# Kernel tuning notes

Measured on AMD Instinct MI355X. Metric: run time of the kernel, lower is better.

Reference implementation:

```python
import jax, jax.numpy as jnp
import numpy as np

N, C, K = 100000, 64, 27
EPS = 1e-5


def setup_inputs() -> dict:
    key = jax.random.key(0)
    ks = jax.random.split(key, 8)
    feats = jax.random.normal(ks[0], (N, C), dtype=jnp.float32)
    W1 = jax.random.normal(ks[1], (K, C, C), dtype=jnp.float32) * (1.0 / np.sqrt(K * C))
    W2 = jax.random.normal(ks[2], (K, C, C), dtype=jnp.float32) * (1.0 / np.sqrt(K * C))
    gamma1 = jnp.ones((C,), dtype=jnp.float32)
    beta1 = jnp.zeros((C,), dtype=jnp.float32)
    gamma2 = jnp.ones((C,), dtype=jnp.float32)
    beta2 = jnp.zeros((C,), dtype=jnp.float32)
    nbr_idx1 = jax.random.randint(ks[3], (K, N), 0, N, dtype=jnp.int32)
    nbr_idx2 = jax.random.randint(ks[4], (K, N), 0, N, dtype=jnp.int32)
    nbr_mask1 = (jax.random.uniform(ks[5], (K, N)) < 0.7).astype(jnp.float32)
    nbr_mask2 = (jax.random.uniform(ks[6], (K, N)) < 0.7).astype(jnp.float32)
    return {"feats": feats, "W1": W1, "gamma1": gamma1, "beta1": beta1,
            "W2": W2, "gamma2": gamma2, "beta2": beta2,
            "nbr_idx1": nbr_idx1, "nbr_mask1": nbr_mask1,
            "nbr_idx2": nbr_idx2, "nbr_mask2": nbr_mask2}


def sparse_conv(f, idx, mask, W):
    # gather per kernel offset: [K, N, C], mask out missing neighbors
    g = f[idx] * mask[..., None]
    # per-offset GEMM and accumulate over offsets -> [N, C_out]
    return jnp.einsum('knc,kcd->nd', g, W)


def batch_norm(x, gamma, beta):
    # MinkowskiBatchNorm (training): stats over all N points, per channel
    mean = jnp.mean(x, axis=0)
    var = jnp.mean(jnp.square(x - mean), axis=0)
    return (x - mean) * jax.lax.rsqrt(var + EPS) * gamma + beta


def reference(feats, W1, gamma1, beta1, W2, gamma2, beta2,
              nbr_idx1, nbr_mask1, nbr_idx2, nbr_mask2):
    out = sparse_conv(feats, nbr_idx1, nbr_mask1, W1)
    out = jax.nn.relu(batch_norm(out, gamma1, beta1))
    out = sparse_conv(out, nbr_idx2, nbr_mask2, W2)
    out = batch_norm(out, gamma2, beta2)
    out = out + feats          # identity residual (stride=1, no downsample)
    return jax.nn.relu(out)
```

## Files before the change

### kernel.cpp

```cpp
#include <hip/hip_runtime.h>
#include <hip/hip_bf16.h>
#include <stdint.h>
#include <stddef.h>

#define N_PTS 100000
#define KOFF 27

typedef __attribute__((ext_vector_type(8))) __bf16 bf16x8;
typedef __attribute__((ext_vector_type(4))) float f32x4;

__device__ inline unsigned short f2bf(float f) {
  union { float f; unsigned u; } x; x.f = f;
  unsigned r = x.u + 0x7fffu + ((x.u >> 16) & 1u);
  return (unsigned short)(r >> 16);
}

__global__ __launch_bounds__(256) void prep_kernel(const float* __restrict__ feats,
                                                   const float* __restrict__ W1,
                                                   const float* __restrict__ W2,
                                                   unsigned short* __restrict__ featsb,
                                                   unsigned short* __restrict__ f2b,
                                                   unsigned short* __restrict__ wf1,
                                                   unsigned short* __restrict__ wf2,
                                                   float* __restrict__ stats) {
  __shared__ float sW[4096];
  int t = threadIdx.x;
  if (blockIdx.x < 54) {
    int which = blockIdx.x & 1;
    int k = blockIdx.x >> 1;
    const float* W = (which ? W2 : W1) + (size_t)k * 4096;
    unsigned short* wf = (which ? wf2 : wf1) + (size_t)k * 4096;
#pragma unroll
    for (int i = 0; i < 4; ++i)
      ((float4*)sW)[t + 256 * i] = ((const float4*)W)[t + 256 * i];
    __syncthreads();
#pragma unroll
    for (int i = 0; i < 16; ++i) {
      int o = i * 256 + t;
      int j = o & 7, l = (o >> 3) & 63, nt = (o >> 9) & 3, kk = (o >> 11) & 1;
      int c = kk * 32 + ((l >> 4) << 3) + j;
      int d = nt * 16 + (l & 15);
      wf[o] = f2bf(sW[c * 64 + d]);
    }
    return;
  }
  int fb = blockIdx.x - 54;
  int NB = gridDim.x - 54;
  const int NF4 = N_PTS * 16;
  for (int i = fb * 256 + t; i < NF4; i += NB * 256) {
    float4 v = ((const float4*)feats)[i];
    ushort4 o;
    o.x = f2bf(v.x); o.y = f2bf(v.y); o.z = f2bf(v.z); o.w = f2bf(v.w);
    ((ushort4*)featsb)[i] = o;
  }
  if (fb == 0) {
    if (t < 256) stats[t] = 0.f;
    uint4 z = make_uint4(0u, 0u, 0u, 0u);
    if (t < 8)            ((uint4*)(featsb + (size_t)N_PTS * 64))[t] = z;
    if (t >= 8 && t < 16) ((uint4*)(f2b    + (size_t)N_PTS * 64))[t - 8] = z;
  }
}

#define MFMA16(a, b, c) __builtin_amdgcn_mfma_f32_16x16x32_bf16(__builtin_bit_cast(bf16x8, a), __builtin_bit_cast(bf16x8, b), c, 0, 0, 0)

#define STEP(Ac0, Ac1, An0, An1, giN, mN, giF, mF, kcur)                        \
  {                                                                             \
    const uint4* bp = wfv + (size_t)(kcur) * 512 + lane;                        \
    uint4 b0 = bp[0],   b1 = bp[64],  b2 = bp[128], b3 = bp[192];               \
    uint4 b4 = bp[256], b5 = bp[320], b6 = bp[384], b7 = bp[448];               \
    {                                                                           \
      int gie = (mN != 0.f) ? giN : N_PTS;                                      \
      const char* rp = (const char*)fin + (size_t)gie * 128 + g16;              \
      An0 = *(const uint4*)rp;                                                  \
      An1 = *(const uint4*)(rp + 64);                                           \
    }                                                                           \
    {                                                                           \
      int kf = ((kcur) + 2 <= 26) ? (kcur) + 2 : 26;                            \
      giF = idxp[(size_t)kf * N_PTS];                                           \
      float mt = mp[(size_t)kf * N_PTS];                                        \
      mF = valid ? mt : 0.f;                                                    \
    }                                                                           \
    a0 = MFMA16(Ac0, b0, a0);                                                   \
    a1 = MFMA16(Ac0, b1, a1);                                                   \
    a2 = MFMA16(Ac0, b2, a2);                                                   \
    a3 = MFMA16(Ac0, b3, a3);                                                   \
    a0 = MFMA16(Ac1, b4, a0);                                                   \
    a1 = MFMA16(Ac1, b5, a1);                                                   \
    a2 = MFMA16(Ac1, b6, a2);                                                   \
    a3 = MFMA16(Ac1, b7, a3);                                                   \
  }

__global__ __launch_bounds__(256, 4) void conv_kernel(
    const unsigned short* __restrict__ fin,
    const unsigned short* __restrict__ wf,
    const int* __restrict__ idx,
    const float* __restrict__ mask,
    float* __restrict__ yout,
    float* __restrict__ gsum,
    float* __restrict__ gsq)
{
  int lane = threadIdx.x & 63;
  int wid  = threadIdx.x >> 6;
  int m    = lane & 15;
  int g    = lane >> 4;
  int g16  = g * 16;
  int n0   = blockIdx.x * 64 + wid * 16;
  int n    = n0 + m;
  bool valid = n < N_PTS;
  int nc = valid ? n : (N_PTS - 1);

  const int*   idxp = idx + nc;
  const float* mp   = mask + nc;
  const uint4* wfv  = (const uint4*)wf;

  f32x4 a0, a1, a2, a3;
#pragma unroll
  for (int r = 0; r < 4; ++r) { a0[r] = 0.f; a1[r] = 0.f; a2[r] = 0.f; a3[r] = 0.f; }

  uint4 Aa0, Aa1, Ab0, Ab1;
  int gi_a, gi_b; float m_a, m_b;

  gi_a = idxp[0];
  { float mt = mp[0]; m_a = valid ? mt : 0.f; }
  {
    int gie = (m_a != 0.f) ? gi_a : N_PTS;
    const char* rp = (const char*)fin + (size_t)gie * 128 + g16;
    Aa0 = *(const uint4*)rp;
    Aa1 = *(const uint4*)(rp + 64);
  }
  gi_b = idxp[N_PTS];
  { float mt = mp[N_PTS]; m_b = valid ? mt : 0.f; }

  for (int kk = 0; kk < 13; ++kk) {
    int k = 2 * kk;
    STEP(Aa0, Aa1, Ab0, Ab1, gi_b, m_b, gi_a, m_a, k);
    STEP(Ab0, Ab1, Aa0, Aa1, gi_a, m_a, gi_b, m_b, k + 1);
  }
  {
    const uint4* bp = wfv + (size_t)26 * 512 + lane;
    uint4 b0 = bp[0],   b1 = bp[64],  b2 = bp[128], b3 = bp[192];
    uint4 b4 = bp[256], b5 = bp[320], b6 = bp[384], b7 = bp[448];
    a0 = MFMA16(Aa0, b0, a0);
    a1 = MFMA16(Aa0, b1, a1);
    a2 = MFMA16(Aa0, b2, a2);
    a3 = MFMA16(Aa0, b3, a3);
    a0 = MFMA16(Aa1, b4, a0);
    a1 = MFMA16(Aa1, b5, a1);
    a2 = MFMA16(Aa1, b6, a2);
    a3 = MFMA16(Aa1, b7, a3);
  }

  __shared__ float s_sum[64], s_sq[64];
  if (threadIdx.x < 64) { s_sum[threadIdx.x] = 0.f; s_sq[threadIdx.x] = 0.f; }
  __syncthreads();

  float s0 = 0.f, q0 = 0.f, s1 = 0.f, q1 = 0.f, s2 = 0.f, q2 = 0.f, s3 = 0.f, q3 = 0.f;
#pragma unroll
  for (int r = 0; r < 4; ++r) {
    int row = n0 + g * 4 + r;
    bool rv = row < N_PTS;
    float v0 = a0[r]; s0 += v0; q0 += v0 * v0;
    float v1 = a1[r]; s1 += v1; q1 += v1 * v1;
    float v2 = a2[r]; s2 += v2; q2 += v2 * v2;
    float v3 = a3[r]; s3 += v3; q3 += v3 * v3;
    if (rv) {
      float* yr = yout + (size_t)row * 64;
      yr[m]      = v0;
      yr[16 + m] = v1;
      yr[32 + m] = v2;
      yr[48 + m] = v3;
    }
  }
  atomicAdd(&s_sum[m],      s0); atomicAdd(&s_sq[m],      q0);
  atomicAdd(&s_sum[16 + m], s1); atomicAdd(&s_sq[16 + m], q1);
  atomicAdd(&s_sum[32 + m], s2); atomicAdd(&s_sq[32 + m], q2);
  atomicAdd(&s_sum[48 + m], s3); atomicAdd(&s_sq[48 + m], q3);
  __syncthreads();
  if (threadIdx.x < 64) {
    atomicAdd(&gsum[threadIdx.x], s_sum[threadIdx.x]);
    atomicAdd(&gsq[threadIdx.x],  s_sq[threadIdx.x]);
  }
}

__global__ void bn1_kernel(const float* __restrict__ y,
                           const float* __restrict__ sum,
                           const float* __restrict__ sq,
                           const float* __restrict__ gamma,
                           const float* __restrict__ beta,
                           unsigned short* __restrict__ outb) {
  __shared__ float s_scale[64], s_shift[64];
  if (threadIdx.x < 64) {
    int c = threadIdx.x;
    float mean = sum[c] * (1.f / N_PTS);
    float var  = sq[c] * (1.f / N_PTS) - mean * mean;
    float inv  = rsqrtf(var + 1e-5f);
    float sc   = gamma[c] * inv;
    s_scale[c] = sc;
    s_shift[c] = beta[c] - mean * sc;
  }
  __syncthreads();
  int tid = blockIdx.x * blockDim.x + threadIdx.x;
  int stride = gridDim.x * blockDim.x;
  const int NT = N_PTS * 16;
  for (int i = tid; i < NT; i += stride) {
    float4 v = ((const float4*)y)[i];
    int c = (i * 4) & 63;
    float r0 = fmaxf(v.x * s_scale[c]     + s_shift[c],     0.f);
    float r1 = fmaxf(v.y * s_scale[c + 1] + s_shift[c + 1], 0.f);
    float r2 = fmaxf(v.z * s_scale[c + 2] + s_shift[c + 2], 0.f);
    float r3 = fmaxf(v.w * s_scale[c + 3] + s_shift[c + 3], 0.f);
    ushort4 o;
    o.x = f2bf(r0); o.y = f2bf(r1); o.z = f2bf(r2); o.w = f2bf(r3);
    ((ushort4*)outb)[i] = o;
  }
}

__global__ void bn2_kernel(const float* __restrict__ y,
                           const float* __restrict__ sum,
                           const float* __restrict__ sq,
                           const float* __restrict__ gamma,
                           const float* __restrict__ beta,
                           const float* __restrict__ feats,
                           float* __restrict__ out) {
  __shared__ float s_scale[64], s_shift[64];
  if (threadIdx.x < 64) {
    int c = threadIdx.x;
    float mean = sum[c] * (1.f / N_PTS);
    float var  = sq[c] * (1.f / N_PTS) - mean * mean;
    float inv  = rsqrtf(var + 1e-5f);
    float sc   = gamma[c] * inv;
    s_scale[c] = sc;
    s_shift[c] = beta[c] - mean * sc;
  }
  __syncthreads();
  int tid = blockIdx.x * blockDim.x + threadIdx.x;
  int stride = gridDim.x * blockDim.x;
  const int NT = N_PTS * 16;
  for (int i = tid; i < NT; i += stride) {
    float4 v = ((const float4*)y)[i];
    float4 f = ((const float4*)feats)[i];
    int c = (i * 4) & 63;
    float4 o;
    o.x = fmaxf(v.x * s_scale[c]     + s_shift[c]     + f.x, 0.f);
    o.y = fmaxf(v.y * s_scale[c + 1] + s_shift[c + 1] + f.y, 0.f);
    o.z = fmaxf(v.z * s_scale[c + 2] + s_shift[c + 2] + f.z, 0.f);
    o.w = fmaxf(v.w * s_scale[c + 3] + s_shift[c + 3] + f.w, 0.f);
    ((float4*)out)[i] = o;
  }
}

extern "C" void kernel_launch(void* const* d_in, const int* in_sizes, int n_in,
                              void* d_out, int out_size, void* d_ws, size_t ws_size,
                              hipStream_t stream) {
  const float* feats  = (const float*)d_in[0];
  const float* W1     = (const float*)d_in[1];
  const float* gamma1 = (const float*)d_in[2];
  const float* beta1  = (const float*)d_in[3];
  const float* W2     = (const float*)d_in[4];
  const float* gamma2 = (const float*)d_in[5];
  const float* beta2  = (const float*)d_in[6];
  const int*   idx1   = (const int*)d_in[7];
  const float* mask1  = (const float*)d_in[8];
  const int*   idx2   = (const int*)d_in[9];
  const float* mask2  = (const float*)d_in[10];
  float* out = (float*)d_out;

  char* ws = (char*)d_ws;
  unsigned short* featsb = (unsigned short*)(ws + 0);
  unsigned short* wf1    = (unsigned short*)(ws + 12800768);
  unsigned short* wf2    = (unsigned short*)(ws + 13021952);
  float*          stats  = (float*)(ws + 13243136);
  unsigned short* f2b    = (unsigned short*)(ws + 13244160);

  float* sum1 = stats;       float* sq1 = stats + 64;
  float* sum2 = stats + 128; float* sq2 = stats + 192;

  float* y = out;

  prep_kernel<<<54 + 640, 256, 0, stream>>>(feats, W1, W2, featsb, f2b, wf1, wf2, stats);

  const int CONV_GRID = (N_PTS + 63) / 64;
  conv_kernel<<<CONV_GRID, 256, 0, stream>>>(featsb, wf1, idx1, mask1, y, sum1, sq1);
  bn1_kernel<<<1024, 256, 0, stream>>>(y, sum1, sq1, gamma1, beta1, f2b);
  conv_kernel<<<CONV_GRID, 256, 0, stream>>>(f2b, wf2, idx2, mask2, y, sum2, sq2);
  bn2_kernel<<<1024, 256, 0, stream>>>(y, sum2, sq2, gamma2, beta2, feats, out);
}
```

Baseline: 349.2 us.

## Stage per-offset weights in double-buffered LDS and process 32 rows per wave

```diff
diff --git a/kernel.cpp b/kernel.cpp
--- a/kernel.cpp
+++ b/kernel.cpp
@@ -63,34 +63,53 @@
 
 #define MFMA16(a, b, c) __builtin_amdgcn_mfma_f32_16x16x32_bf16(__builtin_bit_cast(bf16x8, a), __builtin_bit_cast(bf16x8, b), c, 0, 0, 0)
 
-#define STEP(Ac0, Ac1, An0, An1, giN, mN, giF, mF, kcur)                        \
+#define STEP(kcur, Aca0, Acb0, Aca1, Acb1, Ana0, Anb0, Ana1, Anb1,              \
+             iN0, mN0, iN1, mN1, iF0, mF0, iF1, mF1)                            \
   {                                                                             \
-    const uint4* bp = wfv + (size_t)(kcur) * 512 + lane;                        \
-    uint4 b0 = bp[0],   b1 = bp[64],  b2 = bp[128], b3 = bp[192];               \
-    uint4 b4 = bp[256], b5 = bp[320], b6 = bp[384], b7 = bp[448];               \
-    {                                                                           \
-      int gie = (mN != 0.f) ? giN : N_PTS;                                      \
+    const size_t kn = (size_t)((kcur) + 1) * 8192;                              \
+    S0 = *(const uint4*)(wfB + kn + t16);                                       \
+    S1 = *(const uint4*)(wfB + kn + 4096 + t16);                                \
+    {                                                                           \
+      int gie = (mN0 != 0.f) ? iN0 : N_PTS;                                     \
       const char* rp = (const char*)fin + (size_t)gie * 128 + g16;              \
-      An0 = *(const uint4*)rp;                                                  \
-      An1 = *(const uint4*)(rp + 64);                                           \
+      Ana0 = *(const uint4*)rp; Anb0 = *(const uint4*)(rp + 64);                \
+    }                                                                           \
+    {                                                                           \
+      int gie = (mN1 != 0.f) ? iN1 : N_PTS;                                     \
+      const char* rp = (const char*)fin + (size_t)gie * 128 + g16;              \
+      Ana1 = *(const uint4*)rp; Anb1 = *(const uint4*)(rp + 64);                \
     }                                                                           \
     {                                                                           \
       int kf = ((kcur) + 2 <= 26) ? (kcur) + 2 : 26;                            \
-      giF = idxp[(size_t)kf * N_PTS];                                           \
-      float mt = mp[(size_t)kf * N_PTS];                                        \
-      mF = valid ? mt : 0.f;                                                    \
-    }                                                                           \
-    a0 = MFMA16(Ac0, b0, a0);                                                   \
-    a1 = MFMA16(Ac0, b1, a1);                                                   \
-    a2 = MFMA16(Ac0, b2, a2);                                                   \
-    a3 = MFMA16(Ac0, b3, a3);                                                   \
-    a0 = MFMA16(Ac1, b4, a0);                                                   \
-    a1 = MFMA16(Ac1, b5, a1);                                                   \
-    a2 = MFMA16(Ac1, b6, a2);                                                   \
-    a3 = MFMA16(Ac1, b7, a3);                                                   \
-  }
-
-__global__ __launch_bounds__(256, 4) void conv_kernel(
+      iF0 = idxp0[(size_t)kf * N_PTS];                                          \
+      float mt0 = mp0[(size_t)kf * N_PTS]; mF0 = v0 ? mt0 : 0.f;                \
+      iF1 = idxp1[(size_t)kf * N_PTS];                                          \
+      float mt1 = mp1[(size_t)kf * N_PTS]; mF1 = v1 ? mt1 : 0.f;                \
+    }                                                                           \
+    {                                                                           \
+      const uint4* bL = (const uint4*)sB[cur];                                  \
+      uint4 b0 = bL[lane],       b1 = bL[64 + lane];                            \
+      uint4 b2 = bL[128 + lane], b3 = bL[192 + lane];                           \
+      uint4 b4 = bL[256 + lane], b5 = bL[320 + lane];                           \
+      uint4 b6 = bL[384 + lane], b7 = bL[448 + lane];                           \
+      a00 = MFMA16(Aca0, b0, a00); a01 = MFMA16(Aca0, b1, a01);                 \
+      a02 = MFMA16(Aca0, b2, a02); a03 = MFMA16(Aca0, b3, a03);                 \
+      a10 = MFMA16(Aca1, b0, a10); a11 = MFMA16(Aca1, b1, a11);                 \
+      a12 = MFMA16(Aca1, b2, a12); a13 = MFMA16(Aca1, b3, a13);                 \
+      a00 = MFMA16(Acb0, b4, a00); a01 = MFMA16(Acb0, b5, a01);                 \
+      a02 = MFMA16(Acb0, b6, a02); a03 = MFMA16(Acb0, b7, a03);                 \
+      a10 = MFMA16(Acb1, b4, a10); a11 = MFMA16(Acb1, b5, a11);                 \
+      a12 = MFMA16(Acb1, b6, a12); a13 = MFMA16(Acb1, b7, a13);                 \
+    }                                                                           \
+    {                                                                           \
+      uint4* wL = (uint4*)sB[cur ^ 1];                                          \
+      wL[t] = S0; wL[t + 256] = S1;                                             \
+    }                                                                           \
+    __syncthreads();                                                            \
+    cur ^= 1;                                                                   \
+  }
+
+__global__ __launch_bounds__(256, 3) void conv_kernel(
     const unsigned short* __restrict__ fin,
     const unsigned short* __restrict__ wf,
     const int* __restrict__ idx,
@@ -99,76 +118,111 @@
     float* __restrict__ gsum,
     float* __restrict__ gsq)
 {
-  int lane = threadIdx.x & 63;
-  int wid  = threadIdx.x >> 6;
+  __shared__ __align__(16) unsigned char sB[2][8192];
+  __shared__ float s_sum[64], s_sq[64];
+
+  int t    = threadIdx.x;
+  int lane = t & 63;
+  int wid  = t >> 6;
   int m    = lane & 15;
   int g    = lane >> 4;
   int g16  = g * 16;
-  int n0   = blockIdx.x * 64 + wid * 16;
-  int n    = n0 + m;
-  bool valid = n < N_PTS;
-  int nc = valid ? n : (N_PTS - 1);
-
-  const int*   idxp = idx + nc;
-  const float* mp   = mask + nc;
-  const uint4* wfv  = (const uint4*)wf;
-
-  f32x4 a0, a1, a2, a3;
+  size_t t16 = (size_t)t * 16;
+  int nw   = blockIdx.x * 128 + wid * 32;
+  int n0r  = nw + m;
+  int n1r  = nw + 16 + m;
+  bool v0  = n0r < N_PTS;
+  bool v1  = n1r < N_PTS;
+  int nc0  = v0 ? n0r : 0;
+  int nc1  = v1 ? n1r : 0;
+
+  const int*   idxp0 = idx + nc0;
+  const int*   idxp1 = idx + nc1;
+  const float* mp0   = mask + nc0;
+  const float* mp1   = mask + nc1;
+  const char*  wfB   = (const char*)wf;
+
+  if (t < 64) { s_sum[t] = 0.f; s_sq[t] = 0.f; }
+
+  f32x4 a00, a01, a02, a03, a10, a11, a12, a13;
 #pragma unroll
-  for (int r = 0; r < 4; ++r) { a0[r] = 0.f; a1[r] = 0.f; a2[r] = 0.f; a3[r] = 0.f; }
-
-  uint4 Aa0, Aa1, Ab0, Ab1;
-  int gi_a, gi_b; float m_a, m_b;
-
-  gi_a = idxp[0];
-  { float mt = mp[0]; m_a = valid ? mt : 0.f; }
+  for (int r = 0; r < 4; ++r) {
+    a00[r] = 0.f; a01[r] = 0.f; a02[r] = 0.f; a03[r] = 0.f;
+    a10[r] = 0.f; a11[r] = 0.f; a12[r] = 0.f; a13[r] = 0.f;
+  }
+
+  uint4 Aa0, Ab0, Aa1, Ab1;
+  uint4 Ba0, Bb0, Ba1, Bb1;
+  uint4 S0, S1;
+  int iA0, iA1, iB0, iB1;
+  float mA0, mA1, mB0, mB1;
+  int cur = 0;
+
+  iA0 = idxp0[0]; { float mt = mp0[0]; mA0 = v0 ? mt : 0.f; }
+  iA1 = idxp1[0]; { float mt = mp1[0]; mA1 = v1 ? mt : 0.f; }
+  S0 = *(const uint4*)(wfB + t16);
+  S1 = *(const uint4*)(wfB + 4096 + t16);
   {
-    int gie = (m_a != 0.f) ? gi_a : N_PTS;
+    int gie = (mA0 != 0.f) ? iA0 : N_PTS;
     const char* rp = (const char*)fin + (size_t)gie * 128 + g16;
-    Aa0 = *(const uint4*)rp;
-    Aa1 = *(const uint4*)(rp + 64);
-  }
-  gi_b = idxp[N_PTS];
-  { float mt = mp[N_PTS]; m_b = valid ? mt : 0.f; }
+    Aa0 = *(const uint4*)rp; Ab0 = *(const uint4*)(rp + 64);
+  }
+  {
+    int gie = (mA1 != 0.f) ? iA1 : N_PTS;
+    const char* rp = (const char*)fin + (size_t)gie * 128 + g16;
+    Aa1 = *(const uint4*)rp; Ab1 = *(const uint4*)(rp + 64);
+  }
+  iB0 = idxp0[N_PTS]; { float mt = mp0[N_PTS]; mB0 = v0 ? mt : 0.f; }
+  iB1 = idxp1[N_PTS]; { float mt = mp1[N_PTS]; mB1 = v1 ? mt : 0.f; }
+  {
+    uint4* wL = (uint4*)sB[0];
+    wL[t] = S0; wL[t + 256] = S1;
+  }
+  __syncthreads();
 
   for (int kk = 0; kk < 13; ++kk) {
     int k = 2 * kk;
-    STEP(Aa0, Aa1, Ab0, Ab1, gi_b, m_b, gi_a, m_a, k);
-    STEP(Ab0, Ab1, Aa0, Aa1, gi_a, m_a, gi_b, m_b, k + 1);
-  }
+    STEP(k,     Aa0, Ab0, Aa1, Ab1,  Ba0, Bb0, Ba1, Bb1,
+         iB0, mB0, iB1, mB1,  iA0, mA0, iA1, mA1);
+    STEP(k + 1, Ba0, Bb0, Ba1, Bb1,  Aa0, Ab0, Aa1, Ab1,
+         iA0, mA0, iA1, mA1,  iB0, mB0, iB1, mB1);
+  }
+
   {
-    const uint4* bp = wfv + (size_t)26 * 512 + lane;
-    uint4 b0 = bp[0],   b1 = bp[64],  b2 = bp[128], b3 = bp[192];
-    uint4 b4 = bp[256], b5 = bp[320], b6 = bp[384], b7 = bp[448];
-    a0 = MFMA16(Aa0, b0, a0);
-    a1 = MFMA16(Aa0, b1, a1);
-    a2 = MFMA16(Aa0, b2, a2);
-    a3 = MFMA16(Aa0, b3, a3);
-    a0 = MFMA16(Aa1, b4, a0);
-    a1 = MFMA16(Aa1, b5, a1);
-    a2 = MFMA16(Aa1, b6, a2);
-    a3 = MFMA16(Aa1, b7, a3);
-  }
-
-  __shared__ float s_sum[64], s_sq[64];
-  if (threadIdx.x < 64) { s_sum[threadIdx.x] = 0.f; s_sq[threadIdx.x] = 0.f; }
-  __syncthreads();
-
-  float s0 = 0.f, q0 = 0.f, s1 = 0.f, q1 = 0.f, s2 = 0.f, q2 = 0.f, s3 = 0.f, q3 = 0.f;
+    const uint4* bL = (const uint4*)sB[cur];
+    uint4 b0 = bL[lane],       b1 = bL[64 + lane];
+    uint4 b2 = bL[128 + lane], b3 = bL[192 + lane];
+    uint4 b4 = bL[256 + lane], b5 = bL[320 + lane];
+    uint4 b6 = bL[384 + lane], b7 = bL[448 + lane];
+    a00 = MFMA16(Aa0, b0, a00); a01 = MFMA16(Aa0, b1, a01);
+    a02 = MFMA16(Aa0, b2, a02); a03 = MFMA16(Aa0, b3, a03);
+    a10 = MFMA16(Aa1, b0, a10); a11 = MFMA16(Aa1, b1, a11);
+    a12 = MFMA16(Aa1, b2, a12); a13 = MFMA16(Aa1, b3, a13);
+    a00 = MFMA16(Ab0, b4, a00); a01 = MFMA16(Ab0, b5, a01);
+    a02 = MFMA16(Ab0, b6, a02); a03 = MFMA16(Ab0, b7, a03);
+    a10 = MFMA16(Ab1, b4, a10); a11 = MFMA16(Ab1, b5, a11);
+    a12 = MFMA16(Ab1, b6, a12); a13 = MFMA16(Ab1, b7, a13);
+  }
+
+  float s0 = 0.f, q0 = 0.f, s1 = 0.f, q1 = 0.f;
+  float s2 = 0.f, q2 = 0.f, s3 = 0.f, q3 = 0.f;
 #pragma unroll
   for (int r = 0; r < 4; ++r) {
-    int row = n0 + g * 4 + r;
-    bool rv = row < N_PTS;
-    float v0 = a0[r]; s0 += v0; q0 += v0 * v0;
-    float v1 = a1[r]; s1 += v1; q1 += v1 * v1;
-    float v2 = a2[r]; s2 += v2; q2 += v2 * v2;
-    float v3 = a3[r]; s3 += v3; q3 += v3 * v3;
-    if (rv) {
-      float* yr = yout + (size_t)row * 64;
-      yr[m]      = v0;
-      yr[16 + m] = v1;
-      yr[32 + m] = v2;
-      yr[48 + m] = v3;
+    int row0 = nw + g * 4 + r;
+    int row1 = nw + 16 + g * 4 + r;
+    float u0 = a00[r], u1 = a01[r], u2 = a02[r], u3 = a03[r];
+    float w0 = a10[r], w1 = a11[r], w2 = a12[r], w3 = a13[r];
+    s0 += u0 + w0; q0 += u0 * u0 + w0 * w0;
+    s1 += u1 + w1; q1 += u1 * u1 + w1 * w1;
+    s2 += u2 + w2; q2 += u2 * u2 + w2 * w2;
+    s3 += u3 + w3; q3 += u3 * u3 + w3 * w3;
+    if (row0 < N_PTS) {
+      float* yr = yout + (size_t)row0 * 64;
+      yr[m] = u0; yr[16 + m] = u1; yr[32 + m] = u2; yr[48 + m] = u3;
+    }
+    if (row1 < N_PTS) {
+      float* yr = yout + (size_t)row1 * 64;
+      yr[m] = w0; yr[16 + m] = w1; yr[32 + m] = w2; yr[48 + m] = w3;
     }
   }
   atomicAdd(&s_sum[m],      s0); atomicAdd(&s_sq[m],      q0);
@@ -176,9 +230,9 @@
   atomicAdd(&s_sum[32 + m], s2); atomicAdd(&s_sq[32 + m], q2);
   atomicAdd(&s_sum[48 + m], s3); atomicAdd(&s_sq[48 + m], q3);
   __syncthreads();
-  if (threadIdx.x < 64) {
-    atomicAdd(&gsum[threadIdx.x], s_sum[threadIdx.x]);
-    atomicAdd(&gsq[threadIdx.x],  s_sq[threadIdx.x]);
+  if (t < 64) {
+    atomicAdd(&gsum[t], s_sum[t]);
+    atomicAdd(&gsq[t],  s_sq[t]);
   }
 }
 
@@ -279,7 +333,7 @@
 
   prep_kernel<<<54 + 640, 256, 0, stream>>>(feats, W1, W2, featsb, f2b, wf1, wf2, stats);
 
-  const int CONV_GRID = (N_PTS + 63) / 64;
+  const int CONV_GRID = (N_PTS + 127) / 128;
   conv_kernel<<<CONV_GRID, 256, 0, stream>>>(featsb, wf1, idx1, mask1, y, sum1, sq1);
   bn1_kernel<<<1024, 256, 0, stream>>>(y, sum1, sq1, gamma1, beta1, f2b);
   conv_kernel<<<CONV_GRID, 256, 0, stream>>>(f2b, wf2, idx2, mask2, y, sum2, sq2);
```

New measurement: 300.6 us. 13.9% less time.
